# Kernel optimization log

Measured on AMD Instinct MI355X. Metric: run time of the kernel, lower is better.

The kernel has to match this reference:

```python
import jax, jax.numpy as jnp
import numpy as np

B, N, NE = 16, 96, 256
ATOM, EDIM, HID, LAT, HEADS = 128, 16, 128, 128, 4
HD = LAT // HEADS
RBF, CUT, ZEMB, MAXZ = 16, 5.0, 32, 100
MUL0_IN, MUL1_IN = 64, 32      # irreps_node = 64x0e + 32x1o (dim 160)
MUL0_OUT, MUL1_OUT = 32, 16    # out irreps  = 32x0e + 16x1o (dim 80)
NODE_DIM = MUL0_IN + 3 * MUL1_IN
OUT_DIM = MUL0_OUT + 3 * MUL1_OUT
E_ATT = 1024
WNUM = MUL0_IN*MUL0_OUT + MUL0_IN*MUL1_OUT + MUL1_IN*MUL1_OUT + MUL1_IN*MUL0_OUT  # 4608


def _mlp3(x, w1, b1, w2, b2, w3, b3):
    x = jax.nn.silu(x @ w1 + b1)
    x = jax.nn.silu(x @ w2 + b2)
    return x @ w3 + b3


def setup_inputs() -> dict:
    key = jax.random.key(0)
    ks = jax.random.split(key, 40)
    s = 0.05  # scale params so deep MLP activations stay numerically sane
    d = {}
    d['h'] = jax.random.normal(ks[0], (B, N, ATOM), jnp.float32)
    d['h_full'] = jax.random.normal(ks[1], (B, N, NODE_DIM), jnp.float32)
    d['e_feat'] = jax.random.normal(ks[2], (NE, EDIM), jnp.float32)
    d['att_dist'] = jax.random.uniform(ks[3], (E_ATT,), jnp.float32)
    d['att_vec'] = jax.random.normal(ks[4], (E_ATT, 3), jnp.float32)
    d['z_emb_table'] = jax.random.normal(ks[5], (MAXZ + 1, ZEMB), jnp.float32) * s
    d['rw1'] = jax.random.normal(ks[6], (ZEMB + 1 + RBF, HID), jnp.float32) * s
    d['rb1'] = jnp.zeros((HID,), jnp.float32)
    d['rw2'] = jax.random.normal(ks[7], (HID, WNUM), jnp.float32) * s
    d['rb2'] = jnp.zeros((WNUM,), jnp.float32)
    d['ew1'] = jax.random.normal(ks[8], (EDIM, HID), jnp.float32) * s
    d['eb1'] = jnp.zeros((HID,), jnp.float32)
    d['ew2'] = jax.random.normal(ks[9], (HID, MUL0_OUT + MUL1_OUT), jnp.float32) * s
    d['eb2'] = jnp.zeros((MUL0_OUT + MUL1_OUT,), jnp.float32)
    d['qw1'] = jax.random.normal(ks[10], (ATOM + EDIM, HID), jnp.float32) * s
    d['qb1'] = jnp.zeros((HID,), jnp.float32)
    d['qw2'] = jax.random.normal(ks[11], (HID, HID), jnp.float32) * s
    d['qb2'] = jnp.zeros((HID,), jnp.float32)
    d['qw3'] = jax.random.normal(ks[12], (HID, LAT), jnp.float32) * s
    d['qb3'] = jnp.zeros((LAT,), jnp.float32)
    d['kw1'] = jax.random.normal(ks[13], (ATOM + ZEMB + 1 + RBF, HID), jnp.float32) * s
    d['kb1'] = jnp.zeros((HID,), jnp.float32)
    d['kw2'] = jax.random.normal(ks[14], (HID, HID), jnp.float32) * s
    d['kb2'] = jnp.zeros((HID,), jnp.float32)
    d['kw3'] = jax.random.normal(ks[15], (HID, LAT), jnp.float32) * s
    d['kb3'] = jnp.zeros((LAT,), jnp.float32)
    d['ow1'] = jax.random.normal(ks[16], (MUL0_OUT + MUL1_OUT, HID), jnp.float32) * s
    d['ob1'] = jnp.zeros((HID,), jnp.float32)
    d['ow2'] = jax.random.normal(ks[17], (HID, HID), jnp.float32) * s
    d['ob2'] = jnp.zeros((HID,), jnp.float32)
    d['ow3'] = jax.random.normal(ks[18], (HID, LAT), jnp.float32) * s
    d['ob3'] = jnp.zeros((LAT,), jnp.float32)
    d['z'] = jax.random.randint(ks[19], (B, N), 0, MAXZ)
    d['mask'] = jnp.ones((B, N), bool)
    d['absorber_index'] = jax.random.randint(ks[20], (B,), 0, N)
    d['att_dst'] = jnp.arange(E_ATT)  # unique flat indices into B*N
    return d


def reference(h, h_full, e_feat, att_dist, att_vec, z_emb_table,
              rw1, rb1, rw2, rb2, ew1, eb1, ew2, eb2,
              qw1, qb1, qw2, qb2, qw3, qb3,
              kw1, kb1, kw2, kb2, kw3, kb3,
              ow1, ob1, ow2, ob2, ow3, ob3,
              z, mask, absorber_index, att_dst):
    Bz, Na, Hd = h.shape
    F = Bz * Na
    nE = e_feat.shape[0]
    # scatter edge data into flat (B*N) atom slots
    am_flat = jnp.zeros((F,), bool).at[att_dst].set(True)
    d_flat = jnp.zeros((F,), h.dtype).at[att_dst].set(att_dist)
    v_flat = jnp.zeros((F, 3), h.dtype).at[att_dst].set(att_vec)
    att_mask = am_flat.reshape(Bz, Na) & mask
    # spherical harmonics (lmax=1, component normalization): Y0 = 1, Y1 = sqrt(3)*unit_vec
    un = v_flat / jnp.maximum(jnp.linalg.norm(v_flat, axis=-1, keepdims=True), 1e-8)
    y1 = jnp.sqrt(3.0) * un
    # Gaussian RBF on absorber->atom distance
    mu = jnp.linspace(0.0, CUT, RBF)
    delta = CUT / (RBF - 1)
    rbf = jnp.exp(-(d_flat[:, None] - mu) ** 2 / (2.0 * delta * delta))  # (F, RBF)
    zr = z_emb_table[z]                      # (B, N, ZEMB)
    zr_flat = zr.reshape(F, -1)
    is_abs = jnp.zeros((Bz, Na), h.dtype).at[jnp.arange(Bz), absorber_index].set(1.0)
    # radial MLP -> per-edge tensor-product weights
    w_in = jnp.concatenate([zr_flat, is_abs.reshape(F, 1), rbf], -1)
    tpw = jax.nn.silu(w_in @ rw1 + rb1) @ rw2 + rb2  # (F, WNUM)
    s1 = MUL0_IN * MUL0_OUT
    s2 = s1 + MUL0_IN * MUL1_OUT
    s3 = s2 + MUL1_IN * MUL1_OUT
    w00 = tpw[:, :s1].reshape(F, MUL0_IN, MUL0_OUT)   # 0e x 0e -> 0e
    w01 = tpw[:, s1:s2].reshape(F, MUL0_IN, MUL1_OUT) # 0e x 1o -> 1o
    w10 = tpw[:, s2:s3].reshape(F, MUL1_IN, MUL1_OUT) # 1o x 0e -> 1o
    w11 = tpw[:, s3:].reshape(F, MUL1_IN, MUL0_OUT)   # 1o x 1o -> 0e
    hf = h_full.reshape(F, -1)
    x0 = hf[:, :MUL0_IN]
    x1 = hf[:, MUL0_IN:].reshape(F, MUL1_IN, 3)
    alpha = 1.0 / jnp.sqrt(jnp.float32(MUL0_IN + MUL1_IN))  # path fan-in normalization
    c = 1.0 / jnp.sqrt(3.0)                                  # wigner-3j coeff for l=1 couplings
    out0 = alpha * (jnp.einsum('fi,fio->fo', x0, w00)
                    + c * jnp.einsum('fim,fm,fio->fo', x1, y1, w11))
    out1 = alpha * c * (jnp.einsum('fi,fm,fio->fom', x0, y1, w01)
                        + jnp.einsum('fim,fio->fom', x1, w10))
    v_irrep = jnp.concatenate([out0, out1.reshape(F, 3 * MUL1_OUT)], -1)  # (F, OUT_DIM)
    # cosine cutoff envelope + edge mask
    env = jnp.where(d_flat < CUT, 0.5 * (jnp.cos(jnp.pi * d_flat / CUT) + 1.0), 0.0)
    v_irrep = v_irrep * (am_flat.astype(h.dtype) * env)[:, None]
    # energy-conditioned per-irrep-channel modulation
    gates = jax.nn.silu(e_feat @ ew1 + eb1) @ ew2 + eb2  # (nE, 48)
    g_exp = jnp.concatenate([gates[:, :MUL0_OUT],
                             jnp.repeat(gates[:, MUL0_OUT:], 3, axis=-1)], -1)  # (nE, OUT_DIM)
    v_mod = (v_irrep[:, None, :] * g_exp[None]).reshape(Bz, Na, nE, OUT_DIM)
    # invariant multi-head scoring
    h_abs = h[jnp.arange(Bz), absorber_index]  # (B, H)
    q_in = jnp.concatenate([jnp.broadcast_to(h_abs[:, None], (Bz, nE, Hd)),
                            jnp.broadcast_to(e_feat[None], (Bz, nE, EDIM))], -1)
    q = _mlp3(q_in, qw1, qb1, qw2, qb2, qw3, qb3)  # (B, nE, LAT)
    atom_static = jnp.concatenate([h, zr, is_abs[..., None], rbf.reshape(Bz, Na, RBF)], -1)
    k = _mlp3(atom_static, kw1, kb1, kw2, kb2, kw3, kb3)  # (B, N, LAT)
    qh = q.reshape(Bz, nE, HEADS, HD)
    kh = k.reshape(Bz, Na, HEADS, HD)
    scores = (jnp.einsum('behd,bnhd->benh', qh, kh) * (HD ** -0.5)).mean(-1)  # (B, nE, N)
    m = att_mask[:, None, :]
    scores = jnp.where(m, scores, -1e9)
    attn = jax.nn.softmax(scores, axis=2) * m.astype(h.dtype)
    attn = attn / jnp.maximum(attn.sum(2, keepdims=True), 1e-8)
    out_irrep = jnp.einsum('ben,bnec->bec', attn, v_mod)  # (B, nE, OUT_DIM)
    # invariants: scalars + vector norms
    scal = out_irrep[..., :MUL0_OUT]
    vec = out_irrep[..., MUL0_OUT:].reshape(Bz, nE, MUL1_OUT, 3)
    inv = jnp.concatenate([scal, jnp.sqrt(jnp.sum(vec * vec, -1) + 1e-12)], -1)
    return _mlp3(inv, ow1, ob1, ow2, ob2, ow3, ob3)  # (B, nE, LAT)
```

## Files before the change

### kernel.cpp

```cpp
#include <hip/hip_runtime.h>
#include <hip/hip_fp16.h>
#include <math.h>

#define BB 16
#define NN 96
#define NE 256
#define FF (BB*NN)
#define ATOM 128
#define EDIM 16
#define HID 128
#define LAT 128
#define RBFN 16
#define CUTOFF 5.0f
#define ZEMB 32
#define E_ATT 1024
#define M0I 64
#define M1I 32
#define M0O 32
#define M1O 16
#define NODE_DIM 160
#define OUT_DIM 80
#define INVD 48
#define WNUM 4608
#define SEG1 2048
#define SEG2 3072
#define SEG3 3584

#define S1_EDGE 256
#define S1_Q    512
#define S1_GATE 16
#define S1_TRANS 144
#define STAGE1_BLKS 929

#define TP_BLKS 192
#define SCORE_BLKS 128
#define K2_BLKS (TP_BLKS + SCORE_BLKS)

typedef _Float16 half8_t __attribute__((ext_vector_type(8)));
typedef float float4v __attribute__((ext_vector_type(4)));

__device__ __forceinline__ float silu_f(float x) { return x / (1.0f + expf(-x)); }

__global__ __launch_bounds__(256) void k_stage1(
    const float* __restrict__ h, const float* __restrict__ z_emb, const int* __restrict__ z,
    const int* __restrict__ absorber, const float* __restrict__ e_feat,
    const int* __restrict__ att_dst, const float* __restrict__ att_dist,
    const float* __restrict__ att_vec,
    const float* __restrict__ rw1, const float* __restrict__ rb1,
    const float* __restrict__ kw1, const float* __restrict__ kb1,
    const float* __restrict__ kw2, const float* __restrict__ kb2,
    const float* __restrict__ kw3, const float* __restrict__ kb3,
    const float* __restrict__ qw1, const float* __restrict__ qb1,
    const float* __restrict__ qw2, const float* __restrict__ qb2,
    const float* __restrict__ qw3, const float* __restrict__ qb3,
    const float* __restrict__ ew1, const float* __restrict__ eb1,
    const float* __restrict__ ew2, const float* __restrict__ eb2,
    const float* __restrict__ rw2,
    __half* __restrict__ hiddenH, float* __restrict__ kmatw,
    float* __restrict__ qmat, float* __restrict__ gexp,
    __half* __restrict__ rw2T,
    int* __restrict__ inv, float* __restrict__ y1E, float* __restrict__ envE)
{
    __shared__ float smem[3488];
    int blk = blockIdx.x;
    int t = threadIdx.x;

    if (blk < S1_EDGE) {
        float (*sin1)[184] = (float(*)[184])smem;
        float (*l1S)[128]  = (float(*)[128])(smem + 736);
        float (*l2S)[128]  = (float(*)[128])(smem + 736 + 512);
        int w = t >> 6;
        int c = t & 63;
        int e = blk*4 + w;
        int f = att_dst[e];
        int b = f / NN, nn = f - b*NN;
        float d = att_dist[e];
        {
            float2 hv = *(const float2*)&h[f*ATOM + 2*c];
            sin1[w][2*c] = hv.x; sin1[w][2*c + 1] = hv.y;
        }
        if (c < ZEMB) sin1[w][ATOM + c] = z_emb[z[f]*ZEMB + c];
        if (c >= 32 && c < 48) {
            int j = c - 32;
            const float delta = CUTOFF / (RBFN - 1);
            float diff = d - j*delta;
            sin1[w][ATOM + ZEMB + 1 + j] = expf(-diff*diff / (2.0f*delta*delta));
        }
        if (c == 48) sin1[w][ATOM + ZEMB] = (absorber[b] == nn) ? 1.0f : 0.0f;
        __syncthreads();
        int c2 = 2*c;
        {
            float2 a0 = *(const float2*)&rb1[c2];
            float2 a1 = make_float2(0.f, 0.f);
            #pragma unroll 8
            for (int i = 0; i < 48; i += 2) {
                float x0v = sin1[w][ATOM + i], x1v = sin1[w][ATOM + i + 1];
                float2 w0 = *(const float2*)&rw1[i*HID + c2];
                float2 w1 = *(const float2*)&rw1[(i+1)*HID + c2];
                a0.x += x0v*w0.x; a0.y += x0v*w0.y;
                a1.x += x1v*w1.x; a1.y += x1v*w1.y;
            }
            {
                float x0v = sin1[w][ATOM + 48];
                float2 w0 = *(const float2*)&rw1[48*HID + c2];
                a0.x += x0v*w0.x; a0.y += x0v*w0.y;
            }
            *(__half2*)&hiddenH[e*HID + c2] =
                __floats2half2_rn(silu_f(a0.x + a1.x), silu_f(a0.y + a1.y));
        }
        {
            float2 a0 = *(const float2*)&kb1[c2];
            float2 a1 = make_float2(0.f, 0.f);
            #pragma unroll 8
            for (int i = 0; i < 176; i += 2) {
                float x0v = sin1[w][i], x1v = sin1[w][i + 1];
                float2 w0 = *(const float2*)&kw1[i*HID + c2];
                float2 w1 = *(const float2*)&kw1[(i+1)*HID + c2];
                a0.x += x0v*w0.x; a0.y += x0v*w0.y;
                a1.x += x1v*w1.x; a1.y += x1v*w1.y;
            }
            {
                float x0v = sin1[w][176];
                float2 w0 = *(const float2*)&kw1[176*HID + c2];
                a0.x += x0v*w0.x; a0.y += x0v*w0.y;
            }
            l1S[w][c2] = silu_f(a0.x + a1.x); l1S[w][c2+1] = silu_f(a0.y + a1.y);
        }
        __syncthreads();
        {
            float2 a0 = *(const float2*)&kb2[c2];
            float2 a1 = make_float2(0.f, 0.f);
            #pragma unroll 8
            for (int i = 0; i < HID; i += 2) {
                float x0v = l1S[w][i], x1v = l1S[w][i + 1];
                float2 w0 = *(const float2*)&kw2[i*HID + c2];
                float2 w1 = *(const float2*)&kw2[(i+1)*HID + c2];
                a0.x += x0v*w0.x; a0.y += x0v*w0.y;
                a1.x += x1v*w1.x; a1.y += x1v*w1.y;
            }
            l2S[w][c2] = silu_f(a0.x + a1.x); l2S[w][c2+1] = silu_f(a0.y + a1.y);
        }
        __syncthreads();
        {
            float2 a0 = *(const float2*)&kb3[c2];
            float2 a1 = make_float2(0.f, 0.f);
            #pragma unroll 8
            for (int i = 0; i < HID; i += 2) {
                float x0v = l2S[w][i], x1v = l2S[w][i + 1];
                float2 w0 = *(const float2*)&kw3[i*HID + c2];
                float2 w1 = *(const float2*)&kw3[(i+1)*HID + c2];
                a0.x += x0v*w0.x; a0.y += x0v*w0.y;
                a1.x += x1v*w1.x; a1.y += x1v*w1.y;
            }
            float2 o; o.x = a0.x + a1.x; o.y = a0.y + a1.y;
            *(float2*)&kmatw[f*HID + c2] = o;
        }
    } else if (blk < S1_EDGE + S1_Q) {
        float* hA          = smem;
        float (*ef)[16]    = (float(*)[16])(smem + 128);
        float (*part)[128] = (float(*)[128])(smem + 256);
        float* l1S         = smem + 1280;
        float* l2S         = smem + 2304;
        int idx = blk - S1_EDGE;
        int r0 = idx * 8;
        int b  = r0 >> 8;
        int e8 = r0 & 255;
        if (t < 32) *(float4*)&hA[t*4] = *(const float4*)&h[(b*NN + absorber[b])*ATOM + t*4];
        if (t >= 128 && t < 256) { int e = (t - 128) >> 4, j = t & 15; ef[e][j] = e_feat[(e8 + e)*EDIM + j]; }
        __syncthreads();
        int r = t >> 5, c0 = (t & 31)*4;
        {
            float4 a0 = make_float4(0,0,0,0);
            int k0 = r*16;
            #pragma unroll
            for (int k = 0; k < 16; k++) {
                float hv = hA[k0 + k];
                float4 w0 = *(const float4*)&qw1[(k0 + k)*HID + c0];
                a0.x += hv*w0.x; a0.y += hv*w0.y; a0.z += hv*w0.z; a0.w += hv*w0.w;
            }
            *(float4*)&part[r][c0] = a0;
        }
        __syncthreads();
        {
            float4 s = *(const float4*)&qb1[c0];
            #pragma unroll
            for (int g = 0; g < 8; g++) {
                float4 pg = *(const float4*)&part[g][c0];
                s.x += pg.x; s.y += pg.y; s.z += pg.z; s.w += pg.w;
            }
            #pragma unroll
            for (int j = 0; j < 16; j++) {
                float a = ef[r][j];
                float4 w0 = *(const float4*)&qw1[(ATOM + j)*HID + c0];
                s.x += a*w0.x; s.y += a*w0.y; s.z += a*w0.z; s.w += a*w0.w;
            }
            l1S[r*128 + c0]   = silu_f(s.x); l1S[r*128 + c0+1] = silu_f(s.y);
            l1S[r*128 + c0+2] = silu_f(s.z); l1S[r*128 + c0+3] = silu_f(s.w);
        }
        __syncthreads();
        {
            float4 a0 = *(const float4*)&qb2[c0];
            float4 a1 = make_float4(0,0,0,0);
            #pragma unroll 8
            for (int i = 0; i < HID; i += 2) {
                float x0v = l1S[r*128 + i], x1v = l1S[r*128 + i+1];
                float4 w0 = *(const float4*)&qw2[i*HID + c0];
                float4 w1 = *(const float4*)&qw2[(i+1)*HID + c0];
                a0.x += x0v*w0.x; a0.y += x0v*w0.y; a0.z += x0v*w0.z; a0.w += x0v*w0.w;
                a1.x += x1v*w1.x; a1.y += x1v*w1.y; a1.z += x1v*w1.z; a1.w += x1v*w1.w;
            }
            l2S[r*128 + c0]   = silu_f(a0.x + a1.x); l2S[r*128 + c0+1] = silu_f(a0.y + a1.y);
            l2S[r*128 + c0+2] = silu_f(a0.z + a1.z); l2S[r*128 + c0+3] = silu_f(a0.w + a1.w);
        }
        __syncthreads();
        {
            float4 a0 = *(const float4*)&qb3[c0];
            float4 a1 = make_float4(0,0,0,0);
            #pragma unroll 8
            for (int i = 0; i < HID; i += 2) {
                float x0v = l2S[r*128 + i], x1v = l2S[r*128 + i+1];
                float4 w0 = *(const float4*)&qw3[i*HID + c0];
                float4 w1 = *(const float4*)&qw3[(i+1)*HID + c0];
                a0.x += x0v*w0.x; a0.y += x0v*w0.y; a0.z += x0v*w0.z; a0.w += x0v*w0.w;
                a1.x += x1v*w1.x; a1.y += x1v*w1.y; a1.z += x1v*w1.z; a1.w += x1v*w1.w;
            }
            float4 o;
            o.x = a0.x + a1.x; o.y = a0.y + a1.y; o.z = a0.z + a1.z; o.w = a0.w + a1.w;
            *(float4*)&qmat[(r0 + r)*LAT + c0] = o;
        }
    } else if (blk < S1_EDGE + S1_Q + S1_GATE) {
        float (*ef)[16]   = (float(*)[16])smem;
        float (*l1g)[128] = (float(*)[128])(smem + 256);
        float (*gg)[48]   = (float(*)[48])(smem + 256 + 2048);
        int e0 = (blk - S1_EDGE - S1_Q) * 16;
        { int e = t >> 4, i = t & 15; ef[e][i] = e_feat[(e0 + e)*EDIM + i]; }
        __syncthreads();
        int r = t >> 4, c0 = (t & 15)*8;
        {
            float4 a0 = *(const float4*)&eb1[c0];
            float4 a1 = *(const float4*)&eb1[c0 + 4];
            #pragma unroll
            for (int i = 0; i < EDIM; i++) {
                float a = ef[r][i];
                float4 w0 = *(const float4*)&ew1[i*HID + c0];
                float4 w1 = *(const float4*)&ew1[i*HID + c0 + 4];
                a0.x += a*w0.x; a0.y += a*w0.y; a0.z += a*w0.z; a0.w += a*w0.w;
                a1.x += a*w1.x; a1.y += a*w1.y; a1.z += a*w1.z; a1.w += a*w1.w;
            }
            l1g[r][c0]   = silu_f(a0.x); l1g[r][c0+1] = silu_f(a0.y);
            l1g[r][c0+2] = silu_f(a0.z); l1g[r][c0+3] = silu_f(a0.w);
            l1g[r][c0+4] = silu_f(a1.x); l1g[r][c0+5] = silu_f(a1.y);
            l1g[r][c0+6] = silu_f(a1.z); l1g[r][c0+7] = silu_f(a1.w);
        }
        __syncthreads();
        for (int u = t; u < 16*48; u += 256) {
            int e = u / 48, j = u - 48*(u/48);
            float acc = eb2[j];
            #pragma unroll 4
            for (int i = 0; i < HID; i++) acc += l1g[e][i]*ew2[i*48 + j];
            gg[e][j] = acc;
        }
        __syncthreads();
        for (int u = t; u < 16*80; u += 256) {
            int e = u / 80, cc = u - 80*(u/80);
            gexp[(e0 + e)*OUT_DIM + cc] = (cc < M0O) ? gg[e][cc] : gg[e][M0O + (cc - M0O)/3];
        }
    } else if (blk < S1_EDGE + S1_Q + S1_GATE + S1_TRANS) {
        __half* lds = (__half*)smem;
        int tb = blk - (S1_EDGE + S1_Q + S1_GATE);
        int nt = tb % 72, kt = tb / 72;
        int n0 = nt*64, k0 = kt*64;
        for (int p = 0; p < 16; p++) {
            int idx = t + 256*p;
            int kk = idx >> 6, nn = idx & 63;
            lds[nn*66 + kk] = __float2half(rw2[(k0+kk)*WNUM + n0+nn]);
        }
        __syncthreads();
        for (int p = 0; p < 16; p++) {
            int idx = t + 256*p;
            int nn = idx >> 6, kk = idx & 63;
            rw2T[(n0+nn)*HID + k0+kk] = lds[nn*66 + kk];
        }
    } else {
        for (int p = 0; p < 6; p++) inv[t + 256*p] = -1;
        for (int p = 0; p < 4; p++) {
            int e = t + 256*p;
            float d = att_dist[e];
            envE[e] = (d < CUTOFF) ? 0.5f*(cosf(3.14159265358979323846f*d/CUTOFF) + 1.0f) : 0.0f;
            float vx = att_vec[3*e], vy = att_vec[3*e+1], vz = att_vec[3*e+2];
            float nrm = sqrtf(vx*vx + vy*vy + vz*vz);
            float is = 1.0f / fmaxf(nrm, 1e-8f);
            const float s3 = 1.7320508075688772f;
            y1E[3*e]   = s3*vx*is;
            y1E[3*e+1] = s3*vy*is;
            y1E[3*e+2] = s3*vz*is;
        }
        __syncthreads();
        for (int p = 0; p < 4; p++) { int e = t + 256*p; inv[att_dst[e]] = e; }
    }
}

__global__ __launch_bounds__(256) void k_fuse(
    const __half* __restrict__ hiddenH, const __half* __restrict__ rw2T,
    const float* __restrict__ rb2,
    const float* __restrict__ qmat, const float* __restrict__ kmat,
    const int* __restrict__ inv, const int* __restrict__ att_dst,
    const float* __restrict__ h_full,
    const float* __restrict__ envE, const float* __restrict__ y1E,
    float* __restrict__ virr, float* __restrict__ scoresW)
{
    __shared__ __align__(16) char smemraw[34176];
    float* smem = (float*)smemraw;
    int blk = blockIdx.x;
    int t = threadIdx.x;
    if (blk < TP_BLKS) {
        __half* cS   = (__half*)smemraw;
        float* x0f   = smem + 1088;
        float* x1f   = smem + 2112;
        float* xyf   = smem + 3648;
        float* y1f   = smem + 4160;
        float* envf  = smem + 4224;
        int*   fI    = (int*)(smem + 4240);
        int cls  = blk % 3;
        int tile = blk / 3;
        int e0 = tile * 16;
        if (t < 16) {
            int e = e0 + t;
            fI[t] = att_dst[e];
            envf[t] = envE[e];
            y1f[t*4]   = y1E[3*e];
            y1f[t*4+1] = y1E[3*e+1];
            y1f[t*4+2] = y1E[3*e+2];
        }
        __syncthreads();
        for (int p = 0; p < 10; p++) {
            int idx = t + 256*p;
            int edge = idx / 160, j = idx - 160*edge;
            float v = h_full[fI[edge]*NODE_DIM + j];
            if (j < M0I) x0f[edge*64 + j] = v;
            else         x1f[edge*96 + (j - M0I)] = v;
        }
        __syncthreads();
        for (int p = 0; p < 2; p++) {
            int idx = t + 256*p;
            int edge = idx >> 5, i = idx & 31;
            xyf[edge*32 + i] = x1f[edge*96 + 3*i]*y1f[edge*4]
                             + x1f[edge*96 + 3*i+1]*y1f[edge*4+1]
                             + x1f[edge*96 + 3*i+2]*y1f[edge*4+2];
        }
        __syncthreads();

        int wv = t >> 6;
        int lane = t & 63;
        int mrow = lane & 15, quad = lane >> 4;
        const _Float16* hp = (const _Float16*)hiddenH + (e0 + mrow)*HID + quad*8;
        half8_t af[4];
        #pragma unroll
        for (int kc = 0; kc < 4; kc++) af[kc] = *(const half8_t*)(hp + kc*32);

        int edge = t >> 4, o = t & 15;
        float t00 = 0.f, t11 = 0.f;
        float t01 = 0.f, tm0 = 0.f, tm1 = 0.f, tm2 = 0.f;
        int clsAdd = (cls == 1) ? 1 : 0;

        for (int g = 0; g < 12; g++) {
            #pragma unroll
            for (int sub = 0; sub < 2; sub++) {
                int ntl = 2*wv + sub;
                int j = g*8 + ntl;
                int ntg = (cls == 2) ? (128 + j)
                                     : (2*j + clsAdd + ((j >= 64) ? 96 : 0));
                const _Float16* bp = (const _Float16*)rw2T + (ntg*16 + mrow)*HID + quad*8;
                float4v acc = {0.f, 0.f, 0.f, 0.f};
                #pragma unroll
                for (int kc = 0; kc < 4; kc++) {
                    half8_t bf = *(const half8_t*)(bp + kc*32);
                    acc = __builtin_amdgcn_mfma_f32_16x16x32_f16(af[kc], bf, acc, 0, 0, 0);
                }
                float bias = rb2[ntg*16 + mrow];
                #pragma unroll
                for (int r = 0; r < 4; r++)
                    cS[(quad*4 + r)*136 + ntl*16 + mrow] = __float2half(acc[r] + bias);
            }
            __syncthreads();
            if (cls < 2) {
                if (g < 8) {
                    #pragma unroll
                    for (int nt = 0; nt < 8; nt++) {
                        int j = g*8 + nt;
                        float C = __half2float(cS[edge*136 + nt*16 + o]);
                        t00 += x0f[edge*64 + j]*C;
                    }
                } else {
                    #pragma unroll
                    for (int nt = 0; nt < 8; nt++) {
                        int j = g*8 + nt;
                        float C = __half2float(cS[edge*136 + nt*16 + o]);
                        t11 += xyf[edge*32 + (j - 64)]*C;
                    }
                }
            } else {
                if (g < 8) {
                    #pragma unroll
                    for (int nt = 0; nt < 8; nt++) {
                        int j = g*8 + nt;
                        float C = __half2float(cS[edge*136 + nt*16 + o]);
                        t01 += x0f[edge*64 + j]*C;
                    }
                } else {
                    #pragma unroll
                    for (int nt = 0; nt < 8; nt++) {
                        int j = g*8 + nt;
                        int i = j - 64;
                        float C = __half2float(cS[edge*136 + nt*16 + o]);
                        tm0 += x1f[edge*96 + 3*i]*C;
                        tm1 += x1f[edge*96 + 3*i+1]*C;
                        tm2 += x1f[edge*96 + 3*i+2]*C;
                    }
                }
            }
            __syncthreads();
        }
        const float alpha = 0.10206207261596575f;
        const float ccf   = 0.5773502691896258f;
        int f = fI[edge];
        float env = envf[edge];
        if (cls < 2) {
            virr[f*OUT_DIM + cls*16 + o] = alpha*(t00 + ccf*t11)*env;
        } else {
            float y0 = y1f[edge*4], y1v = y1f[edge*4+1], y2 = y1f[edge*4+2];
            virr[f*OUT_DIM + M0O + 3*o]     = alpha*ccf*(t01*y0 + tm0)*env;
            virr[f*OUT_DIM + M0O + 3*o + 1] = alpha*ccf*(t01*y1v + tm1)*env;
            virr[f*OUT_DIM + M0O + 3*o + 2] = alpha*ccf*(t01*y2 + tm2)*env;
        }
    } else {
        int u = blk - TP_BLKS;
        int b  = u >> 3;
        int e0 = (u & 7) * 32;
        float (*Qs)[132] = (float(*)[132])smem;
        float (*Kt)[132] = (float(*)[132])(smem + 32*132);
        float* mS = smem + 2*32*132;
        for (int p = 0; p < 4; p++) {
            int idx = t + 256*p; int e = idx >> 5, i4 = idx & 31;
            *(float4*)&Qs[e][i4*4] = *(const float4*)&qmat[(b*NE + e0 + e)*LAT + i4*4];
        }
        if (t < NN) mS[t] = ((unsigned)inv[b*NN + t] < E_ATT) ? 1.0f : 0.0f;
        int te = t >> 5, tn = t & 31;
        float acc[4][3] = {};
        for (int nt = 0; nt < 3; nt++) {
            __syncthreads();
            for (int p = 0; p < 4; p++) {
                int idx = t + 256*p; int n = idx >> 5, i4 = idx & 31;
                *(float4*)&Kt[n][i4*4] = *(const float4*)&kmat[(b*NN + nt*32 + n)*LAT + i4*4];
            }
            __syncthreads();
            for (int i = 0; i < LAT; i++) {
                float bv = Kt[tn][i];
                acc[0][nt] += Qs[te*4 + 0][i]*bv;
                acc[1][nt] += Qs[te*4 + 1][i]*bv;
                acc[2][nt] += Qs[te*4 + 2][i]*bv;
                acc[3][nt] += Qs[te*4 + 3][i]*bv;
            }
        }
        const float scale = 0.04419417382415922f;
        #pragma unroll
        for (int j = 0; j < 4; j++)
            #pragma unroll
            for (int jj = 0; jj < 3; jj++) {
                int n = tn + 32*jj;
                float s = (mS[n] != 0.f) ? acc[j][jj]*scale : -1e9f;
                scoresW[((b*NE) + e0 + te*4 + j)*NN + n] = s;
            }
    }
}

__global__ __launch_bounds__(256) void k_attf(
    const float* __restrict__ scoresW, const int* __restrict__ inv,
    const float* __restrict__ virr, const float* __restrict__ gexp,
    const float* __restrict__ ow1, const float* __restrict__ ob1,
    const float* __restrict__ ow2, const float* __restrict__ ob2,
    const float* __restrict__ ow3, const float* __restrict__ ob3,
    float* __restrict__ out)
{
    int b  = blockIdx.x >> 5;
    int e0 = (blockIdx.x & 31) * 8;
    int t = threadIdx.x;
    __shared__ float aS[8][100];
    __shared__ float gS[8][84];
    __shared__ float ocS[8][84];
    __shared__ float mS[NN];
    __shared__ float inS[8][INVD];
    __shared__ float l1S[8][HID];
    __shared__ float l2S[8][HID];

    for (int p = 0; p < 3; p++) {
        int idx = t + 256*p;
        int el = idx / NN, n = idx - NN*(idx/NN);
        aS[el][n] = scoresW[((b*NE) + e0 + el)*NN + n];
    }
    if (t < 160) {
        int el = t / 20, c4 = t - 20*(t/20);
        *(float4*)&gS[el][c4*4] = *(const float4*)&gexp[(e0 + el)*OUT_DIM + c4*4];
    }
    if (t < NN) mS[t] = ((unsigned)inv[b*NN + t] < E_ATT) ? 1.0f : 0.0f;
    __syncthreads();

    {
        int el = t >> 5;
        int ng = t & 31;
        float s0 = aS[el][ng], s1 = aS[el][ng + 32], s2 = aS[el][ng + 64];
        float m0 = mS[ng], m1 = mS[ng + 32], m2 = mS[ng + 64];
        float mx = fmaxf(s0, fmaxf(s1, s2));
        #pragma unroll
        for (int off = 1; off < 32; off <<= 1) mx = fmaxf(mx, __shfl_xor(mx, off));
        float e0v = expf(s0 - mx), e1v = expf(s1 - mx), e2v = expf(s2 - mx);
        float sm = e0v + e1v + e2v;
        #pragma unroll
        for (int off = 1; off < 32; off <<= 1) sm += __shfl_xor(sm, off);
        float r = 1.0f / sm;
        float p0 = m0*e0v*r, p1 = m1*e1v*r, p2 = m2*e2v*r;
        float ss = p0 + p1 + p2;
        #pragma unroll
        for (int off = 1; off < 32; off <<= 1) ss += __shfl_xor(ss, off);
        float is = 1.0f / fmaxf(ss, 1e-8f);
        aS[el][ng]      = p0*is;
        aS[el][ng + 32] = p1*is;
        aS[el][ng + 64] = p2*is;
    }
    __syncthreads();

    if (t < 160) {
        int el = t / 20, c4 = t - 20*(t/20);
        const float* vp = virr + (long)b*NN*OUT_DIM + c4*4;
        float4 acc = make_float4(0,0,0,0);
        #pragma unroll 4
        for (int n = 0; n < NN; n++) {
            float a = aS[el][n];
            float4 v = *(const float4*)&vp[n*OUT_DIM];
            acc.x += a*v.x; acc.y += a*v.y; acc.z += a*v.z; acc.w += a*v.w;
        }
        float4 g = *(float4*)&gS[el][c4*4];
        float4 o; o.x = acc.x*g.x; o.y = acc.y*g.y; o.z = acc.z*g.z; o.w = acc.w*g.w;
        *(float4*)&ocS[el][c4*4] = o;
    }
    __syncthreads();

    for (int u = t; u < 8*INVD; u += 256) {
        int el = u / INVD, j = u - INVD*(u/INVD);
        float val;
        if (j < M0O) val = ocS[el][j];
        else {
            int o = j - M0O;
            float x = ocS[el][M0O + 3*o], y = ocS[el][M0O + 3*o + 1], zz = ocS[el][M0O + 3*o + 2];
            val = sqrtf(x*x + y*y + zz*zz + 1e-12f);
        }
        inS[el][j] = val;
    }
    __syncthreads();

    int r = t >> 5, c0 = (t & 31)*4;
    {
        float4 a0 = *(const float4*)&ob1[c0];
        float4 a1 = make_float4(0,0,0,0);
        #pragma unroll 8
        for (int i = 0; i < INVD; i += 2) {
            float x0v = inS[r][i], x1v = inS[r][i+1];
            float4 w0 = *(const float4*)&ow1[i*HID + c0];
            float4 w1 = *(const float4*)&ow1[(i+1)*HID + c0];
            a0.x += x0v*w0.x; a0.y += x0v*w0.y; a0.z += x0v*w0.z; a0.w += x0v*w0.w;
            a1.x += x1v*w1.x; a1.y += x1v*w1.y; a1.z += x1v*w1.z; a1.w += x1v*w1.w;
        }
        l1S[r][c0]   = silu_f(a0.x + a1.x); l1S[r][c0+1] = silu_f(a0.y + a1.y);
        l1S[r][c0+2] = silu_f(a0.z + a1.z); l1S[r][c0+3] = silu_f(a0.w + a1.w);
    }
    __syncthreads();
    {
        float4 a0 = *(const float4*)&ob2[c0];
        float4 a1 = make_float4(0,0,0,0);
        #pragma unroll 8
        for (int i = 0; i < HID; i += 2) {
            float x0v = l1S[r][i], x1v = l1S[r][i+1];
            float4 w0 = *(const float4*)&ow2[i*HID + c0];
            float4 w1 = *(const float4*)&ow2[(i+1)*HID + c0];
            a0.x += x0v*w0.x; a0.y += x0v*w0.y; a0.z += x0v*w0.z; a0.w += x0v*w0.w;
            a1.x += x1v*w1.x; a1.y += x1v*w1.y; a1.z += x1v*w1.z; a1.w += x1v*w1.w;
        }
        l2S[r][c0]   = silu_f(a0.x + a1.x); l2S[r][c0+1] = silu_f(a0.y + a1.y);
        l2S[r][c0+2] = silu_f(a0.z + a1.z); l2S[r][c0+3] = silu_f(a0.w + a1.w);
    }
    __syncthreads();
    {
        float4 a0 = *(const float4*)&ob3[c0];
        float4 a1 = make_float4(0,0,0,0);
        #pragma unroll 8
        for (int i = 0; i < HID; i += 2) {
            float x0v = l2S[r][i], x1v = l2S[r][i+1];
            float4 w0 = *(const float4*)&ow3[i*HID + c0];
            float4 w1 = *(const float4*)&ow3[(i+1)*HID + c0];
            a0.x += x0v*w0.x; a0.y += x0v*w0.y; a0.z += x0v*w0.z; a0.w += x0v*w0.w;
            a1.x += x1v*w1.x; a1.y += x1v*w1.y; a1.z += x1v*w1.z; a1.w += x1v*w1.w;
        }
        float4 o;
        o.x = a0.x + a1.x; o.y = a0.y + a1.y; o.z = a0.z + a1.z; o.w = a0.w + a1.w;
        *(float4*)&out[((b*NE + e0) + r)*LAT + c0] = o;
    }
}

extern "C" void kernel_launch(void* const* d_in, const int* in_sizes, int n_in,
                              void* d_out, int out_size, void* d_ws, size_t ws_size,
                              hipStream_t stream) {
    const float* h        = (const float*)d_in[0];
    const float* h_full   = (const float*)d_in[1];
    const float* e_feat   = (const float*)d_in[2];
    const float* att_dist = (const float*)d_in[3];
    const float* att_vec  = (const float*)d_in[4];
    const float* z_emb    = (const float*)d_in[5];
    const float* rw1 = (const float*)d_in[6];  const float* rb1 = (const float*)d_in[7];
    const float* rw2 = (const float*)d_in[8];  const float* rb2 = (const float*)d_in[9];
    const float* ew1 = (const float*)d_in[10]; const float* eb1 = (const float*)d_in[11];
    const float* ew2 = (const float*)d_in[12]; const float* eb2 = (const float*)d_in[13];
    const float* qw1 = (const float*)d_in[14]; const float* qb1 = (const float*)d_in[15];
    const float* qw2 = (const float*)d_in[16]; const float* qb2 = (const float*)d_in[17];
    const float* qw3 = (const float*)d_in[18]; const float* qb3 = (const float*)d_in[19];
    const float* kw1 = (const float*)d_in[20]; const float* kb1 = (const float*)d_in[21];
    const float* kw2 = (const float*)d_in[22]; const float* kb2 = (const float*)d_in[23];
    const float* kw3 = (const float*)d_in[24]; const float* kb3 = (const float*)d_in[25];
    const float* ow1 = (const float*)d_in[26]; const float* ob1 = (const float*)d_in[27];
    const float* ow2 = (const float*)d_in[28]; const float* ob2 = (const float*)d_in[29];
    const float* ow3 = (const float*)d_in[30]; const float* ob3 = (const float*)d_in[31];
    const int* z        = (const int*)d_in[32];
    const int* absorber = (const int*)d_in[34];
    const int* att_dst  = (const int*)d_in[35];

    float* ws = (float*)d_ws;
    int*   inv     = (int*)ws;
    float* y1E     = ws + 1536;
    float* envE    = ws + 4608;
    float* kmat    = ws + 5632;
    float* qmat    = ws + 202240;
    float* gexp    = ws + 726528;
    float* virr    = ws + 747008;
    float* scoresW = ws + 904704;
    __half* rw2T   = (__half*)(ws + 3657216);
    __half* hiddenH= (__half*)(ws + 3952128);

    float* out = (float*)d_out;

    k_stage1<<<STAGE1_BLKS, 256, 0, stream>>>(h, z_emb, z, absorber, e_feat,
                                              att_dst, att_dist, att_vec,
                                              rw1, rb1, kw1, kb1, kw2, kb2, kw3, kb3,
                                              qw1, qb1, qw2, qb2, qw3, qb3,
                                              ew1, eb1, ew2, eb2, rw2,
                                              hiddenH, kmat, qmat, gexp, rw2T,
                                              inv, y1E, envE);
    k_fuse<<<K2_BLKS, 256, 0, stream>>>(hiddenH, rw2T, rb2, qmat, kmat, inv,
                                        att_dst, h_full, envE, y1E, virr, scoresW);
    k_attf<<<BB*32, 256, 0, stream>>>(scoresW, inv, virr, gexp,
                                      ow1, ob1, ow2, ob2, ow3, ob3, out);
}
```

Measured before the change: 227.0 us.

## Stage full TP weight tile in LDS and replace block barriers with wave barriers

In the tensor-product blocks, all 96 MFMA output tiles are now computed up front into an enlarged LDS buffer, with one block barrier before the contraction. This replaces the 12-round loop that needed two __syncthreads per round. In the stage-1 edge MLP path, block barriers become wave barriers because each wave only touches its own row. Some loop unroll factors are also raised. LDS use rises to about 62KB per block, which may lower occupancy. The barrier after the h_full gather is removed, so correctness now depends on the later barrier covering those reads.

```diff
diff --git a/kernel.cpp b/kernel.cpp
--- a/kernel.cpp
+++ b/kernel.cpp
@@ -36,6 +36,8 @@
 #define SCORE_BLKS 128
 #define K2_BLKS (TP_BLKS + SCORE_BLKS)
 
+#define CSTR 1544
+
 typedef _Float16 half8_t __attribute__((ext_vector_type(8)));
 typedef float float4v __attribute__((ext_vector_type(4)));
 
@@ -87,7 +89,7 @@
             sin1[w][ATOM + ZEMB + 1 + j] = expf(-diff*diff / (2.0f*delta*delta));
         }
         if (c == 48) sin1[w][ATOM + ZEMB] = (absorber[b] == nn) ? 1.0f : 0.0f;
-        __syncthreads();
+        __builtin_amdgcn_wave_barrier();
         int c2 = 2*c;
         {
             float2 a0 = *(const float2*)&rb1[c2];
@@ -111,7 +113,7 @@
         {
             float2 a0 = *(const float2*)&kb1[c2];
             float2 a1 = make_float2(0.f, 0.f);
-            #pragma unroll 8
+            #pragma unroll 16
             for (int i = 0; i < 176; i += 2) {
                 float x0v = sin1[w][i], x1v = sin1[w][i + 1];
                 float2 w0 = *(const float2*)&kw1[i*HID + c2];
@@ -126,11 +128,11 @@
             }
             l1S[w][c2] = silu_f(a0.x + a1.x); l1S[w][c2+1] = silu_f(a0.y + a1.y);
         }
-        __syncthreads();
+        __builtin_amdgcn_wave_barrier();
         {
             float2 a0 = *(const float2*)&kb2[c2];
             float2 a1 = make_float2(0.f, 0.f);
-            #pragma unroll 8
+            #pragma unroll 16
             for (int i = 0; i < HID; i += 2) {
                 float x0v = l1S[w][i], x1v = l1S[w][i + 1];
                 float2 w0 = *(const float2*)&kw2[i*HID + c2];
@@ -140,11 +142,11 @@
             }
             l2S[w][c2] = silu_f(a0.x + a1.x); l2S[w][c2+1] = silu_f(a0.y + a1.y);
         }
-        __syncthreads();
+        __builtin_amdgcn_wave_barrier();
         {
             float2 a0 = *(const float2*)&kb3[c2];
             float2 a1 = make_float2(0.f, 0.f);
-            #pragma unroll 8
+            #pragma unroll 16
             for (int i = 0; i < HID; i += 2) {
                 float x0v = l2S[w][i], x1v = l2S[w][i + 1];
                 float2 w0 = *(const float2*)&kw3[i*HID + c2];
@@ -309,18 +311,19 @@
     const float* __restrict__ envE, const float* __restrict__ y1E,
     float* __restrict__ virr, float* __restrict__ scoresW)
 {
-    __shared__ __align__(16) char smemraw[34176];
+    __shared__ __align__(16) char smemraw[62208];
     float* smem = (float*)smemraw;
     int blk = blockIdx.x;
     int t = threadIdx.x;
     if (blk < TP_BLKS) {
         __half* cS   = (__half*)smemraw;
-        float* x0f   = smem + 1088;
-        float* x1f   = smem + 2112;
-        float* xyf   = smem + 3648;
-        float* y1f   = smem + 4160;
-        float* envf  = smem + 4224;
-        int*   fI    = (int*)(smem + 4240);
+        float* fbase = (float*)(smemraw + 49408);
+        float* x0f   = fbase;
+        float* x1f   = fbase + 1024;
+        float* xyf   = fbase + 2560;
+        float* y1f   = fbase + 3072;
+        float* envf  = fbase + 3136;
+        int*   fI    = (int*)(fbase + 3152);
         int cls  = blk % 3;
         int tile = blk / 3;
         int e0 = tile * 16;
@@ -348,7 +351,6 @@
                              + x1f[edge*96 + 3*i+1]*y1f[edge*4+1]
                              + x1f[edge*96 + 3*i+2]*y1f[edge*4+2];
         }
-        __syncthreads();
 
         int wv = t >> 6;
         int lane = t & 63;
@@ -358,76 +360,54 @@
         #pragma unroll
         for (int kc = 0; kc < 4; kc++) af[kc] = *(const half8_t*)(hp + kc*32);
 
+        int clsAdd = (cls == 1) ? 1 : 0;
+        #pragma unroll 4
+        for (int jj = 0; jj < 24; jj++) {
+            int j = wv*24 + jj;
+            int ntg = (cls == 2) ? (128 + j)
+                                 : (2*j + clsAdd + ((j >= 64) ? 96 : 0));
+            const _Float16* bp = (const _Float16*)rw2T + (ntg*16 + mrow)*HID + quad*8;
+            float4v acc = {0.f, 0.f, 0.f, 0.f};
+            #pragma unroll
+            for (int kc = 0; kc < 4; kc++) {
+                half8_t bf = *(const half8_t*)(bp + kc*32);
+                acc = __builtin_amdgcn_mfma_f32_16x16x32_f16(af[kc], bf, acc, 0, 0, 0);
+            }
+            float bias = rb2[ntg*16 + mrow];
+            #pragma unroll
+            for (int r = 0; r < 4; r++)
+                cS[(quad*4 + r)*CSTR + j*16 + mrow] = __float2half(acc[r] + bias);
+        }
+        __syncthreads();
+
         int edge = t >> 4, o = t & 15;
-        float t00 = 0.f, t11 = 0.f;
-        float t01 = 0.f, tm0 = 0.f, tm1 = 0.f, tm2 = 0.f;
-        int clsAdd = (cls == 1) ? 1 : 0;
-
-        for (int g = 0; g < 12; g++) {
-            #pragma unroll
-            for (int sub = 0; sub < 2; sub++) {
-                int ntl = 2*wv + sub;
-                int j = g*8 + ntl;
-                int ntg = (cls == 2) ? (128 + j)
-                                     : (2*j + clsAdd + ((j >= 64) ? 96 : 0));
-                const _Float16* bp = (const _Float16*)rw2T + (ntg*16 + mrow)*HID + quad*8;
-                float4v acc = {0.f, 0.f, 0.f, 0.f};
-                #pragma unroll
-                for (int kc = 0; kc < 4; kc++) {
-                    half8_t bf = *(const half8_t*)(bp + kc*32);
-                    acc = __builtin_amdgcn_mfma_f32_16x16x32_f16(af[kc], bf, acc, 0, 0, 0);
-                }
-                float bias = rb2[ntg*16 + mrow];
-                #pragma unroll
-                for (int r = 0; r < 4; r++)
-                    cS[(quad*4 + r)*136 + ntl*16 + mrow] = __float2half(acc[r] + bias);
-            }
-            __syncthreads();
-            if (cls < 2) {
-                if (g < 8) {
-                    #pragma unroll
-                    for (int nt = 0; nt < 8; nt++) {
-                        int j = g*8 + nt;
-                        float C = __half2float(cS[edge*136 + nt*16 + o]);
-                        t00 += x0f[edge*64 + j]*C;
-                    }
-                } else {
-                    #pragma unroll
-                    for (int nt = 0; nt < 8; nt++) {
-                        int j = g*8 + nt;
-                        float C = __half2float(cS[edge*136 + nt*16 + o]);
-                        t11 += xyf[edge*32 + (j - 64)]*C;
-                    }
-                }
-            } else {
-                if (g < 8) {
-                    #pragma unroll
-                    for (int nt = 0; nt < 8; nt++) {
-                        int j = g*8 + nt;
-                        float C = __half2float(cS[edge*136 + nt*16 + o]);
-                        t01 += x0f[edge*64 + j]*C;
-                    }
-                } else {
-                    #pragma unroll
-                    for (int nt = 0; nt < 8; nt++) {
-                        int j = g*8 + nt;
-                        int i = j - 64;
-                        float C = __half2float(cS[edge*136 + nt*16 + o]);
-                        tm0 += x1f[edge*96 + 3*i]*C;
-                        tm1 += x1f[edge*96 + 3*i+1]*C;
-                        tm2 += x1f[edge*96 + 3*i+2]*C;
-                    }
-                }
-            }
-            __syncthreads();
-        }
+        const __half* cRow = cS + edge*CSTR + o;
         const float alpha = 0.10206207261596575f;
         const float ccf   = 0.5773502691896258f;
         int f = fI[edge];
         float env = envf[edge];
         if (cls < 2) {
+            float t00 = 0.f, t11 = 0.f;
+            #pragma unroll 8
+            for (int j = 0; j < 64; j++)
+                t00 += x0f[edge*64 + j]*__half2float(cRow[j*16]);
+            #pragma unroll 8
+            for (int j = 64; j < 96; j++)
+                t11 += xyf[edge*32 + (j - 64)]*__half2float(cRow[j*16]);
             virr[f*OUT_DIM + cls*16 + o] = alpha*(t00 + ccf*t11)*env;
         } else {
+            float t01 = 0.f, tm0 = 0.f, tm1 = 0.f, tm2 = 0.f;
+            #pragma unroll 8
+            for (int j = 0; j < 64; j++)
+                t01 += x0f[edge*64 + j]*__half2float(cRow[j*16]);
+            #pragma unroll 8
+            for (int j = 64; j < 96; j++) {
+                int i = j - 64;
+                float C = __half2float(cRow[j*16]);
+                tm0 += x1f[edge*96 + 3*i]*C;
+                tm1 += x1f[edge*96 + 3*i+1]*C;
+                tm2 += x1f[edge*96 + 3*i+2]*C;
+            }
             float y0 = y1f[edge*4], y1v = y1f[edge*4+1], y2 = y1f[edge*4+2];
             virr[f*OUT_DIM + M0O + 3*o]     = alpha*ccf*(t01*y0 + tm0)*env;
             virr[f*OUT_DIM + M0O + 3*o + 1] = alpha*ccf*(t01*y1v + tm1)*env;
```

Result: no change. 226.4 us (-0.3%).
